# Performance work log

Measured on AMD Instinct MI355X. Metric: run time of the kernel, lower is better.

Reference implementation:

```python
import jax, jax.numpy as jnp
import numpy as np

N = 50000        # nodes
E = 800000       # edges (avg degree 16)
IN = 256         # in_size
H = 4            # heads
C = 32           # out_size per head
NEG_SLOPE = 0.2  # PyG GATConv leaky_relu slope
LN_EPS = 1e-5


def setup_inputs() -> dict:
    key = jax.random.key(0)
    ks = jax.random.split(key, 6)
    x = jax.random.normal(ks[0], (N, IN), dtype=jnp.float32)
    edge_index = jax.random.randint(ks[1], (2, E), 0, N, dtype=jnp.int32)
    W = jax.random.normal(ks[2], (IN, H * C), dtype=jnp.float32) * 0.05
    att_src = jax.random.normal(ks[3], (H, C), dtype=jnp.float32) * 0.05
    att_dst = jax.random.normal(ks[4], (H, C), dtype=jnp.float32) * 0.05
    bias = jnp.zeros((H * C,), dtype=jnp.float32)
    ln_gamma = jnp.ones((H * C,), dtype=jnp.float32)
    ln_beta = jnp.zeros((H * C,), dtype=jnp.float32)
    return {"x": x, "edge_index": edge_index, "W": W, "att_src": att_src,
            "att_dst": att_dst, "bias": bias, "ln_gamma": ln_gamma,
            "ln_beta": ln_beta}


def _segment_softmax(alpha, seg, num_segments):
    # alpha: [E, H], softmax over edges sharing the same destination node.
    amax = jax.ops.segment_max(alpha, seg, num_segments=num_segments)  # [N, H]
    amax = jnp.where(jnp.isfinite(amax), amax, 0.0)  # nodes with no in-edges
    ex = jnp.exp(alpha - amax[seg])
    denom = jax.ops.segment_sum(ex, seg, num_segments=num_segments)    # [N, H]
    return ex / (denom[seg] + 1e-16)


def reference(x, edge_index, W, att_src, att_dst, bias, ln_gamma, ln_beta):
    # --- GATConv (concat=True) ---
    x_lin = (x @ W).reshape(N, H, C)                    # [N, H, C]
    a_src = jnp.sum(x_lin * att_src, axis=-1)           # [N, H]
    a_dst = jnp.sum(x_lin * att_dst, axis=-1)           # [N, H]
    src, dst = edge_index[0], edge_index[1]             # messages src -> dst
    alpha = a_src[src] + a_dst[dst]                     # [E, H]
    alpha = jnp.where(alpha >= 0, alpha, NEG_SLOPE * alpha)
    alpha = _segment_softmax(alpha, dst, N)             # [E, H]
    msg = x_lin[src] * alpha[..., None]                 # [E, H, C]
    out = jax.ops.segment_sum(msg, dst, num_segments=N) # [N, H, C]
    out = out.reshape(N, H * C) + bias                  # [N, H*C]
    # --- LayerNorm over feature dim ---
    mu = jnp.mean(out, axis=-1, keepdims=True)
    var = jnp.mean(jnp.square(out - mu), axis=-1, keepdims=True)
    out = (out - mu) * jax.lax.rsqrt(var + LN_EPS) * ln_gamma + ln_beta
    # --- activation ---
    return jax.nn.relu(out)
```

## Files before the change

### kernel.cpp

```cpp
#include <hip/hip_runtime.h>

#define NNODES 50000
#define NEDGES 800000
#define INFEAT 256
#define HC 128
#define NH 4
#define CPH 32

typedef unsigned int uint32;
typedef unsigned short u16;
typedef short short8 __attribute__((ext_vector_type(8)));
typedef float f32x4 __attribute__((ext_vector_type(4)));

__device__ __forceinline__ float b2f(u16 s) {
    uint32 u = ((uint32)s) << 16;
    return __builtin_bit_cast(float, u);
}
__device__ __forceinline__ u16 f2bf(float x) {
    uint32 u = __builtin_bit_cast(uint32, x);
    uint32 r = (u + 0x7FFFu + ((u >> 16) & 1u)) >> 16;
    return (u16)r;
}
__device__ __forceinline__ uint32 pkh2(float a, float b) {
    _Float16 ha = (_Float16)a, hb = (_Float16)b;
    uint32 ua = (uint32)__builtin_bit_cast(unsigned short, ha);
    uint32 ub = (uint32)__builtin_bit_cast(unsigned short, hb);
    return ua | (ub << 16);
}
__device__ __forceinline__ float h2f(u16 h) {
    return (float)__builtin_bit_cast(_Float16, h);
}
__device__ __forceinline__ bool probe_bf16(const void* gamma) {
    return ((const uint32*)gamma)[0] == 0x3F803F80u;
}

__global__ __launch_bounds__(256) void wtp_kernel(const void* __restrict__ W,
                                                  const void* __restrict__ gm,
                                                  u16* __restrict__ wtp,
                                                  int* __restrict__ count) {
    const bool isbf = probe_bf16(gm);
    int c = blockIdx.x * 256 + threadIdx.x;
    int kt = c >> 9, nt = (c >> 6) & 7, l = c & 63;
    int r = l & 15, quad = l >> 4;
    int n = nt * 16 + r;
    int kbase = kt * 32 + quad * 8;
    u16 vals[8];
#pragma unroll
    for (int j = 0; j < 8; ++j) {
        int k = kbase + j;
        vals[j] = isbf ? ((const u16*)W)[k * HC + n] : f2bf(((const float*)W)[k * HC + n]);
    }
    *(uint4*)(wtp + (size_t)c * 8) = *(const uint4*)vals;
    for (int i = c; i < NNODES; i += 4096) count[i] = 0;
}

__global__ __launch_bounds__(256) void gemm_mfma(const void* __restrict__ x,
                                                 const uint4* __restrict__ wtp,
                                                 const void* __restrict__ att_src,
                                                 const void* __restrict__ att_dst,
                                                 const void* __restrict__ gm,
                                                 u16* __restrict__ xlin,
                                                 float* __restrict__ asrc,
                                                 float* __restrict__ adst) {
    __shared__ uint4 bsm[4096];
    const bool isbf = probe_bf16(gm);
    const int tid = threadIdx.x;
#pragma unroll
    for (int rep = 0; rep < 16; ++rep) bsm[rep * 256 + tid] = wtp[rep * 256 + tid];
    __syncthreads();

    int wave = blockIdx.x * 4 + (tid >> 6);
    int lane = tid & 63;
    int r = lane & 15;
    int quad = lane >> 4;
    int m0 = wave * 16;
    int arow = m0 + r;
    if (arow > NNODES - 1) arow = NNODES - 1;
    const size_t abase = (size_t)arow * INFEAT + quad * 8;

    f32x4 acc[8];
#pragma unroll
    for (int nt = 0; nt < 8; ++nt) acc[nt] = (f32x4){0.f, 0.f, 0.f, 0.f};

#pragma unroll
    for (int kt = 0; kt < 8; ++kt) {
        const int k0 = kt * 32;
        short8 afrag;
        if (isbf) {
            uint4 q = *(const uint4*)((const u16*)x + abase + k0);
            afrag = __builtin_bit_cast(short8, q);
        } else {
            const float* xp = (const float*)x + abase + k0;
            float4 f0 = *(const float4*)xp;
            float4 f1 = *(const float4*)(xp + 4);
            uint4 q;
            q.x = (uint32)f2bf(f0.x) | ((uint32)f2bf(f0.y) << 16);
            q.y = (uint32)f2bf(f0.z) | ((uint32)f2bf(f0.w) << 16);
            q.z = (uint32)f2bf(f1.x) | ((uint32)f2bf(f1.y) << 16);
            q.w = (uint32)f2bf(f1.z) | ((uint32)f2bf(f1.w) << 16);
            afrag = __builtin_bit_cast(short8, q);
        }
#pragma unroll
        for (int nt = 0; nt < 8; ++nt) {
            short8 bfrag = __builtin_bit_cast(short8, bsm[(kt * 8 + nt) * 64 + lane]);
            acc[nt] = __builtin_amdgcn_mfma_f32_16x16x32_bf16(afrag, bfrag, acc[nt], 0, 0, 0);
        }
    }
#pragma unroll
    for (int nt = 0; nt < 8; ++nt) {
#pragma unroll
        for (int reg = 0; reg < 4; ++reg) {
            int grow = m0 + quad * 4 + reg;
            if (grow < NNODES) xlin[(size_t)grow * HC + nt * 16 + r] = f2bf(acc[nt][reg]);
        }
    }

    float asv[8], adv[8];
#pragma unroll
    for (int nt = 0; nt < 8; ++nt) {
        int c = nt * 16 + r;
        if (isbf) {
            asv[nt] = b2f(((const u16*)att_src)[c]);
            adv[nt] = b2f(((const u16*)att_dst)[c]);
        } else {
            asv[nt] = ((const float*)att_src)[c];
            adv[nt] = ((const float*)att_dst)[c];
        }
    }
    float psrc[4][4], pdst[4][4];
#pragma unroll
    for (int h = 0; h < 4; ++h)
#pragma unroll
        for (int reg = 0; reg < 4; ++reg) { psrc[h][reg] = 0.f; pdst[h][reg] = 0.f; }
#pragma unroll
    for (int nt = 0; nt < 8; ++nt) {
        const int h = nt >> 1;
#pragma unroll
        for (int reg = 0; reg < 4; ++reg) {
            psrc[h][reg] = fmaf(acc[nt][reg], asv[nt], psrc[h][reg]);
            pdst[h][reg] = fmaf(acc[nt][reg], adv[nt], pdst[h][reg]);
        }
    }
#pragma unroll
    for (int m = 1; m < 16; m <<= 1) {
#pragma unroll
        for (int h = 0; h < 4; ++h)
#pragma unroll
            for (int reg = 0; reg < 4; ++reg) {
                psrc[h][reg] += __shfl_xor(psrc[h][reg], m);
                pdst[h][reg] += __shfl_xor(pdst[h][reg], m);
            }
    }
#pragma unroll
    for (int reg = 0; reg < 4; ++reg)
#pragma unroll
        for (int h = 0; h < 4; ++h)
            if (r == reg * 4 + h) {
                int grow = m0 + quad * 4 + reg;
                if (grow < NNODES) {
                    asrc[grow * 4 + h] = psrc[h][reg];
                    adst[grow * 4 + h] = pdst[h][reg];
                }
            }
}

__global__ __launch_bounds__(256) void hist_kernel(const int* __restrict__ ei,
                                                   int* __restrict__ count,
                                                   int* __restrict__ rank) {
    int e = blockIdx.x * 256 + threadIdx.x;
    if (e < NEDGES) rank[e] = atomicAdd(&count[ei[NEDGES + e]], 1);
}

__global__ __launch_bounds__(256) void blkred_kernel(const int* __restrict__ count,
                                                     int* __restrict__ blksum) {
    int i = blockIdx.x * 256 + threadIdx.x;
    int v = (i < NNODES) ? count[i] : 0;
#pragma unroll
    for (int m = 1; m < 64; m <<= 1) v += __shfl_xor(v, m);
    __shared__ int s[4];
    if ((threadIdx.x & 63) == 0) s[threadIdx.x >> 6] = v;
    __syncthreads();
    if (threadIdx.x == 0) blksum[blockIdx.x] = s[0] + s[1] + s[2] + s[3];
}

__global__ __launch_bounds__(256) void scanout_kernel(const int* __restrict__ count,
                                                      const int* __restrict__ blksum,
                                                      int* __restrict__ offsets) {
    __shared__ int sb[256];
    __shared__ int sd[256];
    const int nblk = (NNODES + 255) / 256;
    int t = threadIdx.x;
    int bv = (t < nblk) ? blksum[t] : 0;
    sb[t] = bv;
    __syncthreads();
    for (int off = 1; off < 256; off <<= 1) {
        int tv = (t >= off) ? sb[t - off] : 0;
        __syncthreads();
        sb[t] += tv;
        __syncthreads();
    }
    int base = sb[blockIdx.x] - blksum[blockIdx.x];

    int i = blockIdx.x * 256 + t;
    int v = (i < NNODES) ? count[i] : 0;
    sd[t] = v;
    __syncthreads();
    for (int off = 1; off < 256; off <<= 1) {
        int tv = (t >= off) ? sd[t - off] : 0;
        __syncthreads();
        sd[t] += tv;
        __syncthreads();
    }
    if (i < NNODES) offsets[i] = base + sd[t] - v;
    if (i == 0) offsets[NNODES] = NEDGES;
}

__global__ __launch_bounds__(256) void scatter_kernel(const int* __restrict__ ei,
                                                      const int* __restrict__ offsets,
                                                      const int* __restrict__ rank,
                                                      const float* __restrict__ asrc,
                                                      const float* __restrict__ adst,
                                                      uint4* __restrict__ recs) {
    int e = blockIdx.x * 256 + threadIdx.x;
    if (e >= NEDGES) return;
    int s = ei[e];
    int d = ei[NEDGES + e];
    int pos = offsets[d] + rank[e];
    float4 av = *(const float4*)(asrc + s * 4);
    float4 dv = *(const float4*)(adst + d * 4);
    float a0 = av.x + dv.x, a1 = av.y + dv.y, a2 = av.z + dv.z, a3 = av.w + dv.w;
    a0 = (a0 >= 0.f) ? a0 : 0.2f * a0;
    a1 = (a1 >= 0.f) ? a1 : 0.2f * a1;
    a2 = (a2 >= 0.f) ? a2 : 0.2f * a2;
    a3 = (a3 >= 0.f) ? a3 : 0.2f * a3;
    uint4 rec;
    rec.x = (uint32)s;
    rec.y = pkh2(__expf(a0), __expf(a1));
    rec.z = pkh2(__expf(a2), __expf(a3));
    rec.w = 0u;
    recs[pos] = rec;
}

__device__ __forceinline__ float recw(const uint4& r, int h) {
    uint32 wp = (h & 2) ? r.z : r.y;
    u16 wh = (h & 1) ? (u16)(wp >> 16) : (u16)(wp & 0xffffu);
    return h2f(wh);
}

__global__ __launch_bounds__(256) void node_kernel(const u16* __restrict__ xlin,
                                                   const int* __restrict__ offsets,
                                                   const uint4* __restrict__ recs,
                                                   const void* __restrict__ bias,
                                                   const void* __restrict__ gamma,
                                                   const void* __restrict__ beta,
                                                   void* __restrict__ out) {
    const bool isbf = probe_bf16(gamma);
    int node = blockIdx.x * 4 + (threadIdx.x >> 6);
    int lane = threadIdx.x & 63;
    int h = lane >> 4;
    int f2 = lane * 2;
    int start = offsets[node];
    int end = offsets[node + 1];

    float dsum = 0.f, acc0 = 0.f, acc1 = 0.f;
    int i = start;
    for (; i + 7 < end; i += 8) {
        uint4 rr[8];
        uint32 pp[8];
#pragma unroll
        for (int j = 0; j < 8; ++j) rr[j] = recs[i + j];
#pragma unroll
        for (int j = 0; j < 8; ++j) pp[j] = *(const uint32*)(xlin + (size_t)rr[j].x * HC + f2);
#pragma unroll
        for (int j = 0; j < 8; ++j) {
            float w = recw(rr[j], h);
            dsum += w;
            acc0 = fmaf(b2f((u16)(pp[j] & 0xffffu)), w, acc0);
            acc1 = fmaf(b2f((u16)(pp[j] >> 16)), w, acc1);
        }
    }
    for (; i + 3 < end; i += 4) {
        uint4 rr[4];
        uint32 pp[4];
#pragma unroll
        for (int j = 0; j < 4; ++j) rr[j] = recs[i + j];
#pragma unroll
        for (int j = 0; j < 4; ++j) pp[j] = *(const uint32*)(xlin + (size_t)rr[j].x * HC + f2);
#pragma unroll
        for (int j = 0; j < 4; ++j) {
            float w = recw(rr[j], h);
            dsum += w;
            acc0 = fmaf(b2f((u16)(pp[j] & 0xffffu)), w, acc0);
            acc1 = fmaf(b2f((u16)(pp[j] >> 16)), w, acc1);
        }
    }
    for (; i < end; ++i) {
        uint4 r = recs[i];
        float w = recw(r, h);
        uint32 p = *(const uint32*)(xlin + (size_t)r.x * HC + f2);
        dsum += w;
        acc0 = fmaf(b2f((u16)(p & 0xffffu)), w, acc0);
        acc1 = fmaf(b2f((u16)(p >> 16)), w, acc1);
    }
    float rden = 1.f / (dsum + 1e-16f);

    float bi0, bi1, g0, g1, be0, be1;
    if (isbf) {
        uint32 bb = ((const uint32*)bias)[lane];
        uint32 gg = ((const uint32*)gamma)[lane];
        uint32 eb = ((const uint32*)beta)[lane];
        bi0 = b2f((u16)(bb & 0xffffu)); bi1 = b2f((u16)(bb >> 16));
        g0  = b2f((u16)(gg & 0xffffu)); g1  = b2f((u16)(gg >> 16));
        be0 = b2f((u16)(eb & 0xffffu)); be1 = b2f((u16)(eb >> 16));
    } else {
        float2 tb = ((const float2*)bias)[lane];
        float2 tg = ((const float2*)gamma)[lane];
        float2 te = ((const float2*)beta)[lane];
        bi0 = tb.x; bi1 = tb.y; g0 = tg.x; g1 = tg.y; be0 = te.x; be1 = te.y;
    }
    float v0 = fmaf(acc0, rden, bi0);
    float v1 = fmaf(acc1, rden, bi1);
    float s2 = v0 + v1;
    float q2 = v0 * v0 + v1 * v1;
#pragma unroll
    for (int m = 1; m < 64; m <<= 1) {
        s2 += __shfl_xor(s2, m);
        q2 += __shfl_xor(q2, m);
    }
    float mean = s2 * (1.f / 128.f);
    float var = q2 * (1.f / 128.f) - mean * mean;
    float inv = rsqrtf(var + 1e-5f);
    float d0 = v0 - mean, d1 = v1 - mean;
    float o0 = fmaxf(fmaf(d0 * inv, g0, be0), 0.f);
    float o1 = fmaxf(fmaf(d1 * inv, g1, be1), 0.f);
    if (isbf) {
        uint32 po = (uint32)f2bf(o0) | ((uint32)f2bf(o1) << 16);
        ((uint32*)out)[(size_t)node * 64 + lane] = po;
    } else {
        float2 po; po.x = o0; po.y = o1;
        ((float2*)out)[(size_t)node * 64 + lane] = po;
    }
}

extern "C" void kernel_launch(void* const* d_in, const int* in_sizes, int n_in,
                              void* d_out, int out_size, void* d_ws, size_t ws_size,
                              hipStream_t stream) {
    const void* x       = d_in[0];
    const int*  ei      = (const int*)d_in[1];
    const void* W       = d_in[2];
    const void* att_src = d_in[3];
    const void* att_dst = d_in[4];
    const void* bias    = d_in[5];
    const void* gamma   = d_in[6];
    const void* beta    = d_in[7];

    char* w = (char*)d_ws;
    size_t off = 0;
    u16* xlin    = (u16*)(w + off);   off += 12800000;
    u16* wtp     = (u16*)(w + off);   off += 65536;
    float* asrc  = (float*)(w + off); off += 800000;
    float* adst  = (float*)(w + off); off += 800000;
    int* count   = (int*)(w + off);   off += 200000;
    int* offsets = (int*)(w + off);   off += 200016;
    int* rank    = (int*)(w + off);   off += 3200000;
    int* blksum  = (int*)(w + off);   off += 1024;
    uint4* recs  = (uint4*)(w + off); off += 12800000;

    const int NBLK = (NNODES + 255) / 256;
    wtp_kernel<<<16, 256, 0, stream>>>(W, gamma, wtp, count);
    gemm_mfma<<<(NNODES + 63) / 64, 256, 0, stream>>>(x, (const uint4*)wtp, att_src, att_dst,
                                                      gamma, xlin, asrc, adst);
    hist_kernel<<<(NEDGES + 255) / 256, 256, 0, stream>>>(ei, count, rank);
    blkred_kernel<<<NBLK, 256, 0, stream>>>(count, blksum);
    scanout_kernel<<<NBLK, 256, 0, stream>>>(count, blksum, offsets);
    scatter_kernel<<<(NEDGES + 255) / 256, 256, 0, stream>>>(ei, offsets, rank, asrc, adst, recs);
    node_kernel<<<NNODES / 4, 256, 0, stream>>>(xlin, offsets, recs, bias, gamma, beta, d_out);
}
```

Measured before the change: 228.6 us.

## Pack asrc into padded xlin rows and compute edge weights in node kernel

```diff
diff --git a/kernel.cpp b/kernel.cpp
--- a/kernel.cpp
+++ b/kernel.cpp
@@ -6,6 +6,7 @@
 #define HC 128
 #define NH 4
 #define CPH 32
+#define XS 136
 
 typedef unsigned int uint32;
 typedef unsigned short u16;
@@ -20,15 +21,6 @@
     uint32 u = __builtin_bit_cast(uint32, x);
     uint32 r = (u + 0x7FFFu + ((u >> 16) & 1u)) >> 16;
     return (u16)r;
-}
-__device__ __forceinline__ uint32 pkh2(float a, float b) {
-    _Float16 ha = (_Float16)a, hb = (_Float16)b;
-    uint32 ua = (uint32)__builtin_bit_cast(unsigned short, ha);
-    uint32 ub = (uint32)__builtin_bit_cast(unsigned short, hb);
-    return ua | (ub << 16);
-}
-__device__ __forceinline__ float h2f(u16 h) {
-    return (float)__builtin_bit_cast(_Float16, h);
 }
 __device__ __forceinline__ bool probe_bf16(const void* gamma) {
     return ((const uint32*)gamma)[0] == 0x3F803F80u;
@@ -59,16 +51,10 @@
                                                  const void* __restrict__ att_src,
                                                  const void* __restrict__ att_dst,
                                                  const void* __restrict__ gm,
-                                                 u16* __restrict__ xlin,
-                                                 float* __restrict__ asrc,
+                                                 u16* __restrict__ xlinx,
                                                  float* __restrict__ adst) {
-    __shared__ uint4 bsm[4096];
     const bool isbf = probe_bf16(gm);
     const int tid = threadIdx.x;
-#pragma unroll
-    for (int rep = 0; rep < 16; ++rep) bsm[rep * 256 + tid] = wtp[rep * 256 + tid];
-    __syncthreads();
-
     int wave = blockIdx.x * 4 + (tid >> 6);
     int lane = tid & 63;
     int r = lane & 15;
@@ -102,7 +88,7 @@
         }
 #pragma unroll
         for (int nt = 0; nt < 8; ++nt) {
-            short8 bfrag = __builtin_bit_cast(short8, bsm[(kt * 8 + nt) * 64 + lane]);
+            short8 bfrag = __builtin_bit_cast(short8, wtp[(kt * 8 + nt) * 64 + lane]);
             acc[nt] = __builtin_amdgcn_mfma_f32_16x16x32_bf16(afrag, bfrag, acc[nt], 0, 0, 0);
         }
     }
@@ -111,7 +97,7 @@
 #pragma unroll
         for (int reg = 0; reg < 4; ++reg) {
             int grow = m0 + quad * 4 + reg;
-            if (grow < NNODES) xlin[(size_t)grow * HC + nt * 16 + r] = f2bf(acc[nt][reg]);
+            if (grow < NNODES) xlinx[(size_t)grow * XS + nt * 16 + r] = f2bf(acc[nt][reg]);
         }
     }
 
@@ -158,7 +144,7 @@
             if (r == reg * 4 + h) {
                 int grow = m0 + quad * 4 + reg;
                 if (grow < NNODES) {
-                    asrc[grow * 4 + h] = psrc[h][reg];
+                    *(float*)(xlinx + (size_t)grow * XS + 128 + h * 2) = psrc[h][reg];
                     adst[grow * 4 + h] = pdst[h][reg];
                 }
             }
@@ -218,38 +204,17 @@
 __global__ __launch_bounds__(256) void scatter_kernel(const int* __restrict__ ei,
                                                       const int* __restrict__ offsets,
                                                       const int* __restrict__ rank,
-                                                      const float* __restrict__ asrc,
-                                                      const float* __restrict__ adst,
-                                                      uint4* __restrict__ recs) {
+                                                      int* __restrict__ col) {
     int e = blockIdx.x * 256 + threadIdx.x;
     if (e >= NEDGES) return;
-    int s = ei[e];
     int d = ei[NEDGES + e];
-    int pos = offsets[d] + rank[e];
-    float4 av = *(const float4*)(asrc + s * 4);
-    float4 dv = *(const float4*)(adst + d * 4);
-    float a0 = av.x + dv.x, a1 = av.y + dv.y, a2 = av.z + dv.z, a3 = av.w + dv.w;
-    a0 = (a0 >= 0.f) ? a0 : 0.2f * a0;
-    a1 = (a1 >= 0.f) ? a1 : 0.2f * a1;
-    a2 = (a2 >= 0.f) ? a2 : 0.2f * a2;
-    a3 = (a3 >= 0.f) ? a3 : 0.2f * a3;
-    uint4 rec;
-    rec.x = (uint32)s;
-    rec.y = pkh2(__expf(a0), __expf(a1));
-    rec.z = pkh2(__expf(a2), __expf(a3));
-    rec.w = 0u;
-    recs[pos] = rec;
-}
-
-__device__ __forceinline__ float recw(const uint4& r, int h) {
-    uint32 wp = (h & 2) ? r.z : r.y;
-    u16 wh = (h & 1) ? (u16)(wp >> 16) : (u16)(wp & 0xffffu);
-    return h2f(wh);
-}
-
-__global__ __launch_bounds__(256) void node_kernel(const u16* __restrict__ xlin,
+    col[offsets[d] + rank[e]] = ei[e];
+}
+
+__global__ __launch_bounds__(256) void node_kernel(const u16* __restrict__ xlinx,
+                                                   const float* __restrict__ adst,
                                                    const int* __restrict__ offsets,
-                                                   const uint4* __restrict__ recs,
+                                                   const int* __restrict__ col,
                                                    const void* __restrict__ bias,
                                                    const void* __restrict__ gamma,
                                                    const void* __restrict__ beta,
@@ -259,48 +224,46 @@
     int lane = threadIdx.x & 63;
     int h = lane >> 4;
     int f2 = lane * 2;
+    float adh = adst[node * 4 + h];
     int start = offsets[node];
     int end = offsets[node + 1];
 
     float dsum = 0.f, acc0 = 0.f, acc1 = 0.f;
     int i = start;
     for (; i + 7 < end; i += 8) {
-        uint4 rr[8];
-        uint32 pp[8];
-#pragma unroll
-        for (int j = 0; j < 8; ++j) rr[j] = recs[i + j];
-#pragma unroll
-        for (int j = 0; j < 8; ++j) pp[j] = *(const uint32*)(xlin + (size_t)rr[j].x * HC + f2);
+        size_t bb[8];
+        uint32 pf[8];
+        float aw[8];
+#pragma unroll
+        for (int j = 0; j < 8; ++j) bb[j] = (size_t)col[i + j] * XS;
 #pragma unroll
         for (int j = 0; j < 8; ++j) {
-            float w = recw(rr[j], h);
+            pf[j] = *(const uint32*)(xlinx + bb[j] + f2);
+            aw[j] = *(const float*)(xlinx + bb[j] + 128 + h * 2);
+        }
+#pragma unroll
+        for (int j = 0; j < 8; ++j) {
+            float a = aw[j] + adh;
+            a = (a >= 0.f) ? a : 0.2f * a;
+            float w = __expf(a);
             dsum += w;
-            acc0 = fmaf(b2f((u16)(pp[j] & 0xffffu)), w, acc0);
-            acc1 = fmaf(b2f((u16)(pp[j] >> 16)), w, acc1);
-        }
-    }
-    for (; i + 3 < end; i += 4) {
-        uint4 rr[4];
-        uint32 pp[4];
-#pragma unroll
-        for (int j = 0; j < 4; ++j) rr[j] = recs[i + j];
-#pragma unroll
-        for (int j = 0; j < 4; ++j) pp[j] = *(const uint32*)(xlin + (size_t)rr[j].x * HC + f2);
-#pragma unroll
-        for (int j = 0; j < 4; ++j) {
-            float w = recw(rr[j], h);
-            dsum += w;
-            acc0 = fmaf(b2f((u16)(pp[j] & 0xffffu)), w, acc0);
-            acc1 = fmaf(b2f((u16)(pp[j] >> 16)), w, acc1);
+            float x0 = __builtin_bit_cast(float, pf[j] << 16);
+            float x1 = __builtin_bit_cast(float, pf[j] & 0xffff0000u);
+            acc0 = fmaf(x0, w, acc0);
+            acc1 = fmaf(x1, w, acc1);
         }
     }
     for (; i < end; ++i) {
-        uint4 r = recs[i];
-        float w = recw(r, h);
-        uint32 p = *(const uint32*)(xlin + (size_t)r.x * HC + f2);
+        size_t bb = (size_t)col[i] * XS;
+        uint32 p = *(const uint32*)(xlinx + bb + f2);
+        float a = *(const float*)(xlinx + bb + 128 + h * 2) + adh;
+        a = (a >= 0.f) ? a : 0.2f * a;
+        float w = __expf(a);
         dsum += w;
-        acc0 = fmaf(b2f((u16)(p & 0xffffu)), w, acc0);
-        acc1 = fmaf(b2f((u16)(p >> 16)), w, acc1);
+        float x0 = __builtin_bit_cast(float, p << 16);
+        float x1 = __builtin_bit_cast(float, p & 0xffff0000u);
+        acc0 = fmaf(x0, w, acc0);
+        acc1 = fmaf(x1, w, acc1);
     }
     float rden = 1.f / (dsum + 1e-16f);
 
@@ -356,23 +319,23 @@
 
     char* w = (char*)d_ws;
     size_t off = 0;
-    u16* xlin    = (u16*)(w + off);   off += 12800000;
+    u16* xlinx   = (u16*)(w + off);   off += 13600000;
     u16* wtp     = (u16*)(w + off);   off += 65536;
-    float* asrc  = (float*)(w + off); off += 800000;
     float* adst  = (float*)(w + off); off += 800000;
     int* count   = (int*)(w + off);   off += 200000;
     int* offsets = (int*)(w + off);   off += 200016;
     int* rank    = (int*)(w + off);   off += 3200000;
     int* blksum  = (int*)(w + off);   off += 1024;
-    uint4* recs  = (uint4*)(w + off); off += 12800000;
+    int* col     = (int*)(w + off);   off += 3200000;
 
     const int NBLK = (NNODES + 255) / 256;
     wtp_kernel<<<16, 256, 0, stream>>>(W, gamma, wtp, count);
     gemm_mfma<<<(NNODES + 63) / 64, 256, 0, stream>>>(x, (const uint4*)wtp, att_src, att_dst,
-                                                      gamma, xlin, asrc, adst);
+                                                      gamma, xlinx, adst);
     hist_kernel<<<(NEDGES + 255) / 256, 256, 0, stream>>>(ei, count, rank);
     blkred_kernel<<<NBLK, 256, 0, stream>>>(count, blksum);
     scanout_kernel<<<NBLK, 256, 0, stream>>>(count, blksum, offsets);
-    scatter_kernel<<<(NEDGES + 255) / 256, 256, 0, stream>>>(ei, offsets, rank, asrc, adst, recs);
-    node_kernel<<<NNODES / 4, 256, 0, stream>>>(xlin, offsets, recs, bias, gamma, beta, d_out);
-}
+    scatter_kernel<<<(NEDGES + 255) / 256, 256, 0, stream>>>(ei, offsets, rank, col);
+    node_kernel<<<NNODES / 4, 256, 0, stream>>>(xlinx, adst, offsets, col,
+                                                bias, gamma, beta, d_out);
+}
```

Measured after the change: 228.5 us. Within noise of the previous version (-0.0%).
